# Kernel optimization log

Measured on AMD Instinct MI355X. Metric: run time of the kernel, lower is better.

The kernel has to match this reference:

```python
import jax, jax.numpy as jnp
import numpy as np
from jax import lax

CLIP = 10.0


def setup_inputs() -> dict:
    key = jax.random.key(0)
    k1, k2, k3, k4 = jax.random.split(key, 4)
    B, T, I, H = 64, 512, 512, 512
    x = jax.random.normal(k1, (B, T, I), dtype=jnp.float32)
    kernel = jax.random.normal(k2, (I, H), dtype=jnp.float32) * 0.05
    recurrent_kernel = jax.random.normal(k3, (H, H), dtype=jnp.float32) * 0.05
    bias_i = jax.random.normal(k4, (H,), dtype=jnp.float32) * 0.05
    h0 = jnp.zeros((B, H), dtype=jnp.float32)
    return {"x": x, "kernel": kernel, "recurrent_kernel": recurrent_kernel,
            "bias_i": bias_i, "h0": h0}


def reference(x, kernel, recurrent_kernel, bias_i, h0):
    # Elman RNN: Ht = tanh(clip(Xt@W + Ht-1@R + b, -clip, clip))
    def step(h, xt):
        g = xt @ kernel + h @ recurrent_kernel + bias_i  # [B, H]
        h_new = jnp.tanh(jnp.clip(g, -CLIP, CLIP))
        return h_new, h_new

    xs = jnp.swapaxes(x, 0, 1)  # [T, B, I] for scan over time
    h_last, ys = lax.scan(step, h0, xs)
    outputs = jnp.swapaxes(ys, 0, 1)  # [B, T, H]
    return outputs, h_last
```

## Files before the change

kernel.cpp:

```cpp
#include <hip/hip_runtime.h>

#define Bdim 64
#define Tdim 512
#define Idim 512
#define Hdim 512
#define CLIPV 10.0f
#define NREGP 46
#define NLDSP 18

typedef __attribute__((ext_vector_type(4))) float f32x4;
typedef __attribute__((ext_vector_type(8))) short bf16x8;
typedef _Float16 half2v __attribute__((ext_vector_type(2)));

__device__ __forceinline__ ushort f2bf(float f) {
    unsigned u = __builtin_bit_cast(unsigned, f);
    u += 0x7fffu + ((u >> 16) & 1u);
    return (ushort)(u >> 16);
}
__device__ __forceinline__ float bf2f(ushort h) {
    return __builtin_bit_cast(float, (unsigned)h << 16);
}
__device__ __forceinline__ void split_bf(float f, ushort& h, ushort& l) {
    h = f2bf(f);
    l = f2bf(f - bf2f(h));
}
__device__ __forceinline__ float dot2acc(uint r, uint h2, float acc) {
#if __has_builtin(__builtin_amdgcn_fdot2)
    return __builtin_amdgcn_fdot2(__builtin_bit_cast(half2v, r),
                                  __builtin_bit_cast(half2v, h2), acc, false);
#else
    half2v a = __builtin_bit_cast(half2v, r);
    half2v b = __builtin_bit_cast(half2v, h2);
    return acc + (float)a.x * (float)b.x + (float)a.y * (float)b.y;
#endif
}
__device__ __forceinline__ uint packf16(float a, float b) {
    _Float16 fa = (_Float16)a, fb = (_Float16)b;
    return (uint)__builtin_bit_cast(ushort, fa) |
           ((uint)__builtin_bit_cast(ushort, fb) << 16);
}
__device__ __forceinline__ ushort f2h(float f) {
    _Float16 h = (_Float16)f;
    return __builtin_bit_cast(ushort, h);
}
__device__ __forceinline__ float fastrcp(float x) {
#if __has_builtin(__builtin_amdgcn_rcpf)
    return __builtin_amdgcn_rcpf(x);
#else
    return 1.0f / x;
#endif
}

__global__ __launch_bounds__(256) void transpose_w_kernel(const float* __restrict__ w,
                                                          ushort* __restrict__ wth,
                                                          ushort* __restrict__ wtl) {
    int idx = blockIdx.x * 256 + threadIdx.x;
    int k = idx >> 9, n = idx & 511;
    ushort h, l;
    split_bf(w[idx], h, l);
    wth[n * Idim + k] = h;
    wtl[n * Idim + k] = l;
}

__global__ __launch_bounds__(256) void pack_r_kernel(const float* __restrict__ Rw,
                                                     uint* __restrict__ rpk) {
    int d = blockIdx.x * 256 + threadIdx.x;
    int i = d >> 11;
    int rem = d & 2047;
    int t = rem >> 2, q = rem & 3;
    int k = (t >> 7) * 128 + 2 * i;
    int c = ((t & 127) << 2) + q;
    rpk[d] = packf16(Rw[(size_t)k * Hdim + c], Rw[(size_t)(k + 1) * Hdim + c]);
}

#define BM 128
#define BN 128
#define BK 32
__global__ __launch_bounds__(256) void gemm_xw(
    const float* __restrict__ A,
    const ushort* __restrict__ Bth,
    const ushort* __restrict__ Btl,
    const float* __restrict__ bias,
    float* __restrict__ C,
    int M, int N, int K)
{
    __shared__ ushort AsH[BM][BK];
    __shared__ ushort AsL[BM][BK];
    __shared__ ushort BsH[BN][BK];
    __shared__ ushort BsL[BN][BK];
    int bm = blockIdx.x, bn = blockIdx.y;
    int tid = threadIdx.x;
    int wave = tid >> 6, lane = tid & 63;
    int wr = wave >> 1, wc = wave & 1;
    f32x4 acc[4][4] = {};
    const int row0 = bm * BM, col0 = bn * BN;
    const int sr = tid >> 1;
    const int sc = (tid & 1) * 16;

    for (int kt = 0; kt < K; kt += BK) {
        const float* gA = A + (size_t)(row0 + sr) * K + kt + sc;
        #pragma unroll
        for (int q = 0; q < 4; ++q) {
            float4 v = *(const float4*)(gA + q * 4);
            ushort4 h4, l4;
            split_bf(v.x, h4.x, l4.x);
            split_bf(v.y, h4.y, l4.y);
            split_bf(v.z, h4.z, l4.z);
            split_bf(v.w, h4.w, l4.w);
            *(ushort4*)&AsH[sr][sc + q * 4] = h4;
            *(ushort4*)&AsL[sr][sc + q * 4] = l4;
        }
        const int4* gBh = (const int4*)(Bth + (size_t)(col0 + sr) * K + kt + sc);
        *(int4*)&BsH[sr][sc]     = gBh[0];
        *(int4*)&BsH[sr][sc + 8] = gBh[1];
        const int4* gBl = (const int4*)(Btl + (size_t)(col0 + sr) * K + kt + sc);
        *(int4*)&BsL[sr][sc]     = gBl[0];
        *(int4*)&BsL[sr][sc + 8] = gBl[1];
        __syncthreads();

        const int r = lane & 15, kg = lane >> 4;
        bf16x8 ah[4], al[4], bh[4], bl[4];
        #pragma unroll
        for (int m = 0; m < 4; ++m) {
            ah[m] = *(const bf16x8*)&AsH[wr * 64 + m * 16 + r][kg * 8];
            al[m] = *(const bf16x8*)&AsL[wr * 64 + m * 16 + r][kg * 8];
        }
        #pragma unroll
        for (int n = 0; n < 4; ++n) {
            bh[n] = *(const bf16x8*)&BsH[wc * 64 + n * 16 + r][kg * 8];
            bl[n] = *(const bf16x8*)&BsL[wc * 64 + n * 16 + r][kg * 8];
        }
        #pragma unroll
        for (int m = 0; m < 4; ++m)
            #pragma unroll
            for (int n = 0; n < 4; ++n) {
                acc[m][n] = __builtin_amdgcn_mfma_f32_16x16x32_bf16(ah[m], bh[n], acc[m][n], 0, 0, 0);
                acc[m][n] = __builtin_amdgcn_mfma_f32_16x16x32_bf16(ah[m], bl[n], acc[m][n], 0, 0, 0);
                acc[m][n] = __builtin_amdgcn_mfma_f32_16x16x32_bf16(al[m], bh[n], acc[m][n], 0, 0, 0);
            }
        __syncthreads();
    }

    const int cl = lane & 15, rg = lane >> 4;
    #pragma unroll
    for (int n = 0; n < 4; ++n) {
        int gc = col0 + wc * 64 + n * 16 + cl;
        float bv = bias[gc];
        #pragma unroll
        for (int m = 0; m < 4; ++m) {
            int gr = row0 + wr * 64 + m * 16 + rg * 4;
            #pragma unroll
            for (int r2 = 0; r2 < 4; ++r2)
                C[(size_t)(gr + r2) * N + gc] = acc[m][n][r2] + bv;
        }
    }
}

__global__ __launch_bounds__(512, 2) void rnn_reg_kernel(
    const uint* __restrict__ Rpk,
    float* __restrict__ out,
    float* __restrict__ hlast,
    const float* __restrict__ h0)
{
    __shared__ uint Rlds[NLDSP * 2048];
    __shared__ ushort h1[Hdim];
    __shared__ float part[4][Hdim];

    const int tid  = threadIdx.x;
    const int row  = blockIdx.x;
    const int kq   = tid >> 7;
    const int lane = tid & 63;
    const int c0   = (tid & 127) * 4;
    const int hb   = kq * 64;

    uint4 rr4[NREGP];
    const uint* rbase = Rpk + tid * 4;
    #pragma unroll
    for (int i = 0; i < NREGP; ++i)
        rr4[i] = *(const uint4*)(rbase + i * 2048);
    #pragma unroll
    for (int ip = 0; ip < NLDSP; ++ip)
        *(uint4*)&Rlds[ip * 2048 + tid * 4] =
            *(const uint4*)(rbase + (NREGP + ip) * 2048);

    h1[tid] = f2h(h0[row * Hdim + tid]);
    __syncthreads();

    float* orow = out + (size_t)row * Tdim * Hdim;

    for (int t = 0; t < Tdim; ++t, orow += Hdim) {
        float pre = orow[tid];
        uint hval = ((const uint*)h1)[hb + lane];

        float a0 = 0.f, a1 = 0.f, a2 = 0.f, a3 = 0.f;
        #pragma unroll
        for (int i = 0; i < NLDSP; ++i) {
            uint hvi = __builtin_amdgcn_readlane(hval, NREGP + i);
            uint4 rv = *(const uint4*)&Rlds[i * 2048 + tid * 4];
            a0 = dot2acc(rv.x, hvi, a0);
            a1 = dot2acc(rv.y, hvi, a1);
            a2 = dot2acc(rv.z, hvi, a2);
            a3 = dot2acc(rv.w, hvi, a3);
        }
        #pragma unroll
        for (int i = 0; i < NREGP; ++i) {
            uint hvi = __builtin_amdgcn_readlane(hval, i);
            uint4 rv = rr4[i];
            a0 = dot2acc(rv.x, hvi, a0);
            a1 = dot2acc(rv.y, hvi, a1);
            a2 = dot2acc(rv.z, hvi, a2);
            a3 = dot2acc(rv.w, hvi, a3);
        }
        *(f32x4*)&part[kq][c0] = (f32x4){a0, a1, a2, a3};
        __syncthreads();

        float s = part[0][tid] + part[1][tid] + part[2][tid] + part[3][tid] + pre;
        s = fminf(fmaxf(s, -CLIPV), CLIPV);
        float e = __expf(2.0f * s);
        float v = (e - 1.0f) * fastrcp(e + 1.0f);
        orow[tid] = v;
        h1[tid] = f2h(v);
        if (t == Tdim - 1) hlast[row * Hdim + tid] = v;
        __syncthreads();
    }
}

extern "C" void kernel_launch(void* const* d_in, const int* in_sizes, int n_in,
                              void* d_out, int out_size, void* d_ws, size_t ws_size,
                              hipStream_t stream) {
    const float* x    = (const float*)d_in[0];
    const float* W    = (const float*)d_in[1];
    const float* R    = (const float*)d_in[2];
    const float* bias = (const float*)d_in[3];
    const float* h0   = (const float*)d_in[4];
    float* out = (float*)d_out;

    ushort* wth = (ushort*)d_ws;
    ushort* wtl = wth + (size_t)Idim * Hdim;
    uint* rpk   = (uint*)((char*)d_ws + (1u << 20));

    transpose_w_kernel<<<(Idim * Hdim + 255) / 256, 256, 0, stream>>>(W, wth, wtl);
    pack_r_kernel<<<512, 256, 0, stream>>>(R, rpk);

    dim3 gg(Bdim * Tdim / BM, Hdim / BN);
    gemm_xw<<<gg, 256, 0, stream>>>(x, wth, wtl, bias, out, Bdim * Tdim, Hdim, Idim);

    rnn_reg_kernel<<<Bdim, 512, 0, stream>>>(
        rpk, out, out + (size_t)Bdim * Tdim * Hdim, h0);
}
```

Baseline: 834.2 us.

## Repartition recurrent matvec by wave K-slices and drop second barrier via double-buffered partials

```diff
diff --git a/kernel.cpp b/kernel.cpp
--- a/kernel.cpp
+++ b/kernel.cpp
@@ -5,8 +5,8 @@
 #define Idim 512
 #define Hdim 512
 #define CLIPV 10.0f
-#define NREGP 46
-#define NLDSP 18
+#define NREGG 50
+#define NLDSG 14
 
 typedef __attribute__((ext_vector_type(4))) float f32x4;
 typedef __attribute__((ext_vector_type(8))) short bf16x8;
@@ -65,12 +65,14 @@
 __global__ __launch_bounds__(256) void pack_r_kernel(const float* __restrict__ Rw,
                                                      uint* __restrict__ rpk) {
     int d = blockIdx.x * 256 + threadIdx.x;
-    int i = d >> 11;
+    int g = d >> 11;
     int rem = d & 2047;
-    int t = rem >> 2, q = rem & 3;
-    int k = (t >> 7) * 128 + 2 * i;
-    int c = ((t & 127) << 2) + q;
-    rpk[d] = packf16(Rw[(size_t)k * Hdim + c], Rw[(size_t)(k + 1) * Hdim + c]);
+    int t = rem >> 2, r = rem & 3;
+    int j = g >> 1, half = g & 1;
+    int kp = (t >> 6) * 32 + j;
+    int c  = (t & 63) * 8 + half * 4 + r;
+    rpk[d] = packf16(Rw[(size_t)(2 * kp) * Hdim + c],
+                     Rw[(size_t)(2 * kp + 1) * Hdim + c]);
 }
 
 #define BM 128
@@ -162,26 +164,25 @@
     float* __restrict__ hlast,
     const float* __restrict__ h0)
 {
-    __shared__ uint Rlds[NLDSP * 2048];
+    __shared__ uint Rlds[NLDSG * 2048];
     __shared__ ushort h1[Hdim];
-    __shared__ float part[4][Hdim];
-
-    const int tid  = threadIdx.x;
-    const int row  = blockIdx.x;
-    const int kq   = tid >> 7;
-    const int lane = tid & 63;
-    const int c0   = (tid & 127) * 4;
-    const int hb   = kq * 64;
-
-    uint4 rr4[NREGP];
+    __shared__ float part[2][8][Hdim];
+
+    const int tid = threadIdx.x;
+    const int row = blockIdx.x;
+    const int w   = tid >> 6;
+    const int l   = tid & 63;
+    const int col = w * 64 + l;
+
+    uint4 rr4[NREGG];
     const uint* rbase = Rpk + tid * 4;
     #pragma unroll
-    for (int i = 0; i < NREGP; ++i)
+    for (int i = 0; i < NREGG; ++i)
         rr4[i] = *(const uint4*)(rbase + i * 2048);
     #pragma unroll
-    for (int ip = 0; ip < NLDSP; ++ip)
-        *(uint4*)&Rlds[ip * 2048 + tid * 4] =
-            *(const uint4*)(rbase + (NREGP + ip) * 2048);
+    for (int g = 0; g < NLDSG; ++g)
+        *(uint4*)&Rlds[g * 2048 + tid * 4] =
+            *(const uint4*)(rbase + (NREGG + g) * 2048);
 
     h1[tid] = f2h(h0[row * Hdim + tid]);
     __syncthreads();
@@ -189,39 +190,52 @@
     float* orow = out + (size_t)row * Tdim * Hdim;
 
     for (int t = 0; t < Tdim; ++t, orow += Hdim) {
-        float pre = orow[tid];
-        uint hval = ((const uint*)h1)[hb + lane];
+        float pre = orow[col];
+        uint hval = ((const uint*)h1)[w * 32 + (l & 31)];
 
         float a0 = 0.f, a1 = 0.f, a2 = 0.f, a3 = 0.f;
-        #pragma unroll
-        for (int i = 0; i < NLDSP; ++i) {
-            uint hvi = __builtin_amdgcn_readlane(hval, NREGP + i);
-            uint4 rv = *(const uint4*)&Rlds[i * 2048 + tid * 4];
-            a0 = dot2acc(rv.x, hvi, a0);
-            a1 = dot2acc(rv.y, hvi, a1);
-            a2 = dot2acc(rv.z, hvi, a2);
-            a3 = dot2acc(rv.w, hvi, a3);
-        }
-        #pragma unroll
-        for (int i = 0; i < NREGP; ++i) {
-            uint hvi = __builtin_amdgcn_readlane(hval, i);
-            uint4 rv = rr4[i];
-            a0 = dot2acc(rv.x, hvi, a0);
-            a1 = dot2acc(rv.y, hvi, a1);
-            a2 = dot2acc(rv.z, hvi, a2);
-            a3 = dot2acc(rv.w, hvi, a3);
-        }
-        *(f32x4*)&part[kq][c0] = (f32x4){a0, a1, a2, a3};
+        float a4 = 0.f, a5 = 0.f, a6 = 0.f, a7 = 0.f;
+        #pragma unroll
+        for (int j = 0; j < NREGG / 2; ++j) {
+            uint hvi = __builtin_amdgcn_readlane(hval, j);
+            uint4 rA = rr4[2 * j], rB = rr4[2 * j + 1];
+            a0 = dot2acc(rA.x, hvi, a0);
+            a1 = dot2acc(rA.y, hvi, a1);
+            a2 = dot2acc(rA.z, hvi, a2);
+            a3 = dot2acc(rA.w, hvi, a3);
+            a4 = dot2acc(rB.x, hvi, a4);
+            a5 = dot2acc(rB.y, hvi, a5);
+            a6 = dot2acc(rB.z, hvi, a6);
+            a7 = dot2acc(rB.w, hvi, a7);
+        }
+        #pragma unroll
+        for (int j = 0; j < NLDSG / 2; ++j) {
+            uint hvi = __builtin_amdgcn_readlane(hval, NREGG / 2 + j);
+            uint4 rA = *(const uint4*)&Rlds[(2 * j) * 2048 + tid * 4];
+            uint4 rB = *(const uint4*)&Rlds[(2 * j + 1) * 2048 + tid * 4];
+            a0 = dot2acc(rA.x, hvi, a0);
+            a1 = dot2acc(rA.y, hvi, a1);
+            a2 = dot2acc(rA.z, hvi, a2);
+            a3 = dot2acc(rA.w, hvi, a3);
+            a4 = dot2acc(rB.x, hvi, a4);
+            a5 = dot2acc(rB.y, hvi, a5);
+            a6 = dot2acc(rB.z, hvi, a6);
+            a7 = dot2acc(rB.w, hvi, a7);
+        }
+        const int p = t & 1;
+        *(f32x4*)&part[p][w][l * 8]     = (f32x4){a0, a1, a2, a3};
+        *(f32x4*)&part[p][w][l * 8 + 4] = (f32x4){a4, a5, a6, a7};
         __syncthreads();
 
-        float s = part[0][tid] + part[1][tid] + part[2][tid] + part[3][tid] + pre;
+        float s = pre;
+        #pragma unroll
+        for (int e = 0; e < 8; ++e) s += part[p][e][col];
         s = fminf(fmaxf(s, -CLIPV), CLIPV);
-        float e = __expf(2.0f * s);
-        float v = (e - 1.0f) * fastrcp(e + 1.0f);
-        orow[tid] = v;
-        h1[tid] = f2h(v);
-        if (t == Tdim - 1) hlast[row * Hdim + tid] = v;
-        __syncthreads();
+        float e2 = __expf(2.0f * s);
+        float v = (e2 - 1.0f) * fastrcp(e2 + 1.0f);
+        orow[col] = v;
+        h1[col] = f2h(v);
+        if (t == Tdim - 1) hlast[row * Hdim + col] = v;
     }
 }
 
```

After: 780.9 us. 1.07x faster.
